# Optimization experiments

Hardware: AMD Instinct MI355X
Metric: run time of the kernel (lower is better)

Reference implementation:

```python
import jax, jax.numpy as jnp
import numpy as np

B, T, P, W = 32, 4096, 512, 1024  # batch, time, param_size, width


def setup_inputs() -> dict:
    key = jax.random.key(0)
    ks = jax.random.split(key, 9)
    lim = 1.0 / np.sqrt(W).astype(np.float32)
    lim = float(lim)
    u = lambda k, shape, l: jax.random.uniform(k, shape, minval=-l, maxval=l, dtype=jnp.float32)
    a = jax.random.normal(ks[0], (B, T, P), dtype=jnp.float32)
    h0 = u(ks[1], (W,), lim)
    weight_ih = u(ks[2], (3 * W, P), lim)
    weight_hh = u(ks[3], (3 * W, W), lim)
    bias = u(ks[4], (3 * W,), lim)
    bias_n = u(ks[5], (W,), lim)
    lim_o = float(1.0 / np.sqrt(W))
    w_out = u(ks[6], (P, W), lim_o)
    b_out = u(ks[7], (P,), lim_o)
    return {"a": a, "h0": h0, "weight_ih": weight_ih, "weight_hh": weight_hh,
            "bias": bias, "bias_n": bias_n, "w_out": w_out, "b_out": b_out}


def _encode(a, h0, weight_ih, weight_hh, bias, bias_n, w_out, b_out):
    # Precompute input gates for all steps (big GEMM, hoisted out of the scan).
    # ig: [B, T, 3W]
    ig = jnp.einsum('btp,gp->btg', a, weight_ih) + bias

    def step(h, ig_t):
        # h: [B, W], ig_t: [B, 3W]
        hg = h @ weight_hh.T                       # [B, 3W]
        ig_r, ig_z, ig_n = jnp.split(ig_t, 3, axis=-1)
        hg_r, hg_z, hg_n = jnp.split(hg, 3, axis=-1)
        r = jax.nn.sigmoid(ig_r + hg_r)
        z = jax.nn.sigmoid(ig_z + hg_z)
        n = jnp.tanh(ig_n + r * (hg_n + bias_n))
        h_new = n + z * (h - n)                    # equinox GRUCell update
        return h_new, h_new

    h_init = jnp.broadcast_to(h0, (a.shape[0], h0.shape[0]))
    # scan over time (reverse), batched inside: xs [T, B, 3W]
    _, hs = jax.lax.scan(step, h_init, jnp.swapaxes(ig, 0, 1), reverse=True)
    hs = jnp.swapaxes(hs, 0, 1)                    # [B, T, W]
    return hs @ w_out.T + b_out                    # [B, T, P]


def reference(a, h0, weight_ih, weight_hh, bias, bias_n, w_out, b_out):
    return _encode(a, h0, weight_ih, weight_hh, bias, bias_n, w_out, b_out)
```

## Files before the change

### kernel.cpp

```cpp
#include <hip/hip_runtime.h>
#include <cstddef>

#define TT 4096
#define PP 512
#define WW 1024

using u32 = unsigned;
using u64 = unsigned long long;
using u16 = unsigned short;

typedef short short8 __attribute__((ext_vector_type(8)));
typedef float f32x4 __attribute__((ext_vector_type(4)));

__device__ __forceinline__ u32 bfround(float f) {
    u32 u = __float_as_uint(f);
    return (u + 0x7fffu + ((u >> 16) & 1u)) >> 16;
}
__device__ __forceinline__ float bf2f(u32 q) { return __uint_as_float(q << 16); }
__device__ __forceinline__ float bflo(u32 q) { return __uint_as_float(q << 16); }
__device__ __forceinline__ float bfhi(u32 q) { return __uint_as_float(q & 0xffff0000u); }

#define LDA64(p)    __hip_atomic_load((p),  __ATOMIC_RELAXED, __HIP_MEMORY_SCOPE_AGENT)
#define STA64(p, v) __hip_atomic_store((p), (v), __ATOMIC_RELAXED, __HIP_MEMORY_SCOPE_AGENT)
#define LDA32(p)    __hip_atomic_load((p),  __ATOMIC_RELAXED, __HIP_MEMORY_SCOPE_AGENT)
#define STA32(p, v) __hip_atomic_store((p), (v), __ATOMIC_RELAXED, __HIP_MEMORY_SCOPE_AGENT)
#define STA16(p, v) __hip_atomic_store((p), (v), __ATOMIC_RELAXED, __HIP_MEMORY_SCOPE_AGENT)

__global__ __launch_bounds__(256, 2) void a2bf_t(const float* __restrict__ a,
                                                 u16* __restrict__ abf2) {
    __shared__ u16 sh[32][528];

    const int t   = blockIdx.x;
    const int tid = threadIdx.x;

    {
        const int b = tid >> 3, seg = tid & 7;
        const float* ap = &a[((size_t)b * TT + t) * PP + seg * 64];
        #pragma unroll
        for (int j = 0; j < 16; ++j) {
            float4 v = *(const float4*)&ap[j * 4];
            uint2 w;
            w.x = bfround(v.x) | (bfround(v.y) << 16);
            w.y = bfround(v.z) | (bfround(v.w) << 16);
            *(uint2*)&sh[b][seg * 64 + j * 4] = w;
        }
    }
    __syncthreads();
    {
        const int d = tid >> 2, bq = tid & 3;
        #pragma unroll
        for (int bb = 0; bb < 8; ++bb) {
            const int b = bq * 8 + bb;
            uint4 v = *(const uint4*)&sh[b][d * 8];
            *(uint4*)&abf2[(((size_t)t * 64 + d) * 32 + b) * 8] = v;
        }
    }
}

__global__ __launch_bounds__(768, 1) void ig_prepass9(
    const u16* __restrict__ abf2, const float* __restrict__ Wih,
    const float* __restrict__ bias, char* __restrict__ igbase)
{
    const int gp  = blockIdx.x;
    const int t0  = blockIdx.y * 64;
    const int tid = threadIdx.x;
    const int lane = tid & 63;
    const int wid  = tid >> 6;
    const int lq   = lane >> 4;
    const int bcol = lane & 15;

    short8 af[2][16];
    float  bi[2][4];
    int    gWGv[2], slotv[2];
    #pragma unroll
    for (int rt2 = 0; rt2 < 2; ++rt2) {
        const int rowb = gp * 384 + rt2 * 192 + wid * 16;
        const float* wr = &Wih[(size_t)(rowb + bcol) * PP + lq * 8];
        #pragma unroll
        for (int s = 0; s < 16; ++s) {
            float t8[8];
            *(float4*)&t8[0] = *(const float4*)&wr[s * 32];
            *(float4*)&t8[4] = *(const float4*)&wr[s * 32 + 4];
            #pragma unroll
            for (int j = 0; j < 8; ++j) af[rt2][s][j] = (short)bfround(t8[j]);
        }
        const int grow0 = rowb + lq * 4;
        #pragma unroll
        for (int r = 0; r < 4; ++r) bi[rt2][r] = bias[grow0 + r];
        const int gate = grow0 >> 10, w = grow0 & 1023;
        gWGv[rt2]  = w >> 4;
        slotv[rt2] = gate * 16 + (w & 15);
    }

    for (int ct = 0; ct < 128; ++ct) {
        const int t = t0 + (ct >> 1);
        const int b = (ct & 1) * 16 + bcol;
        const u16* bp = &abf2[(((size_t)t * 64 + lq) * 32 + b) * 8];
        f32x4 d0 = {0.f, 0.f, 0.f, 0.f}, d1 = {0.f, 0.f, 0.f, 0.f};
        #pragma unroll 4
        for (int s = 0; s < 16; ++s) {
            short8 bf = *(const short8*)&bp[(size_t)s * 4 * 256];
            d0 = __builtin_amdgcn_mfma_f32_16x16x32_bf16(af[0][s], bf, d0, 0, 0, 0);
            d1 = __builtin_amdgcn_mfma_f32_16x16x32_bf16(af[1][s], bf, d1, 0, 0, 0);
        }
        u32 l0 = bfround(d0[0] + bi[0][0]) | (bfround(d0[1] + bi[0][1]) << 16);
        u32 h0_ = bfround(d0[2] + bi[0][2]) | (bfround(d0[3] + bi[0][3]) << 16);
        u32 l1 = bfround(d1[0] + bi[1][0]) | (bfround(d1[1] + bi[1][1]) << 16);
        u32 h1_ = bfround(d1[2] + bi[1][2]) | (bfround(d1[3] + bi[1][3]) << 16);
        *(u64*)(igbase + (((size_t)t * 64 + gWGv[0]) * 1536 + (size_t)b * 48 + slotv[0]) * 2) = (u64)l0 | ((u64)h0_ << 32);
        *(u64*)(igbase + (((size_t)t * 64 + gWGv[1]) * 1536 + (size_t)b * 48 + slotv[1]) * 2) = (u64)l1 | ((u64)h1_ << 32);
    }
}

__global__ __launch_bounds__(768, 1) void ig_prepass16(
    const float* __restrict__ a, const float* __restrict__ Wih,
    const float* __restrict__ bias, char* __restrict__ igbase)
{
    const int gp   = blockIdx.x;
    const int t0   = blockIdx.y * 64;
    const int tid  = threadIdx.x;
    const int lane = tid & 63;
    const int wid  = tid >> 6;
    const int growb = gp * 192 + wid * 16;

    short8 afrag[16];
    float  biasv[4];
    {
        const float* wr = &Wih[(size_t)(growb + (lane & 15)) * PP + (lane >> 4) * 8];
        #pragma unroll
        for (int s = 0; s < 16; ++s) {
            float t8[8];
            *(float4*)&t8[0] = *(const float4*)&wr[s * 32];
            *(float4*)&t8[4] = *(const float4*)&wr[s * 32 + 4];
            #pragma unroll
            for (int j = 0; j < 8; ++j) afrag[s][j] = (short)bfround(t8[j]);
        }
        #pragma unroll
        for (int r = 0; r < 4; ++r) biasv[r] = bias[growb + (lane >> 4) * 4 + r];
    }
    const int grow0 = growb + (lane >> 4) * 4;
    const int gate  = grow0 >> 10;
    const int w     = grow0 & 1023;
    const int gWG   = w >> 4;
    const int slot  = gate * 16 + (w & 15);
    const int bcol  = lane & 15;

    for (int ct = 0; ct < 128; ++ct) {
        const int t = t0 + (ct >> 1);
        const int b = (ct & 1) * 16 + bcol;
        const float* ap = &a[((size_t)b * TT + t) * PP + (lane >> 4) * 8];
        f32x4 d = {0.f, 0.f, 0.f, 0.f};
        #pragma unroll 4
        for (int s = 0; s < 16; ++s) {
            float4 lo = *(const float4*)&ap[s * 32];
            float4 hi = *(const float4*)&ap[s * 32 + 4];
            short8 bfv;
            bfv[0] = (short)((__float_as_uint(lo.x) + 0x8000u) >> 16);
            bfv[1] = (short)((__float_as_uint(lo.y) + 0x8000u) >> 16);
            bfv[2] = (short)((__float_as_uint(lo.z) + 0x8000u) >> 16);
            bfv[3] = (short)((__float_as_uint(lo.w) + 0x8000u) >> 16);
            bfv[4] = (short)((__float_as_uint(hi.x) + 0x8000u) >> 16);
            bfv[5] = (short)((__float_as_uint(hi.y) + 0x8000u) >> 16);
            bfv[6] = (short)((__float_as_uint(hi.z) + 0x8000u) >> 16);
            bfv[7] = (short)((__float_as_uint(hi.w) + 0x8000u) >> 16);
            d = __builtin_amdgcn_mfma_f32_16x16x32_bf16(afrag[s], bfv, d, 0, 0, 0);
        }
        u32 lo32 = bfround(d[0] + biasv[0]) | (bfround(d[1] + biasv[1]) << 16);
        u32 hi32 = bfround(d[2] + biasv[2]) | (bfround(d[3] + biasv[3]) << 16);
        *(u64*)(igbase + (((size_t)t * 64 + gWG) * 1536 + (size_t)b * 48 + slot) * 2) =
            (u64)lo32 | ((u64)hi32 << 32);
    }
}

__global__ __launch_bounds__(768, 1) void gru_scan4(
    const float* __restrict__ h0v, const float* __restrict__ Whh,
    const float* __restrict__ bias_n, const float* __restrict__ Wout,
    const float* __restrict__ bout, const char* __restrict__ igbase,
    float* __restrict__ out, u64* __restrict__ bufA, u64* __restrict__ bufB,
    u32* __restrict__ flags)
{
    __shared__ float sPreH[4][48][2][17];
    __shared__ float sOutP[4][16][18];
    __shared__ __align__(8) u64 sIgRaw[384];

    const int g    = blockIdx.x;
    const int tid  = threadIdx.x;
    const int lane = tid & 63;
    const int wid  = tid >> 6;
    const int p0   = (g >> 1) * 16;
    const int pb0  = (g & 1) * 16;

    short8 frag[24];
    if (wid < 8) {
        const int kq = wid & 3;
        #pragma unroll
        for (int gate = 0; gate < 3; ++gate)
            #pragma unroll
            for (int s = 0; s < 8; ++s) {
                const float* wr = &Whh[(size_t)(gate * WW + g * 16 + (lane & 15)) * WW
                                       + (kq * 8 + s) * 32 + (lane >> 4) * 8];
                float t8[8];
                *(float4*)&t8[0] = *(const float4*)&wr[0];
                *(float4*)&t8[4] = *(const float4*)&wr[4];
                short8 v;
                #pragma unroll
                for (int j = 0; j < 8; ++j) v[j] = (short)bfround(t8[j]);
                frag[gate * 8 + s] = v;
            }
    } else {
        const int kq3 = wid - 8;
        #pragma unroll
        for (int s = 0; s < 8; ++s) {
            const float* wr = &Wout[(size_t)(p0 + (lane & 15)) * WW
                                    + (kq3 * 8 + s) * 32 + (lane >> 4) * 8];
            float t8[8];
            *(float4*)&t8[0] = *(const float4*)&wr[0];
            *(float4*)&t8[4] = *(const float4*)&wr[4];
            short8 v;
            #pragma unroll
            for (int j = 0; j < 8; ++j) v[j] = (short)bfround(t8[j]);
            frag[s] = v;
        }
    }

    float h_own = 0.f, bnv = 0.f;
    int gwl = 0, gb = 0; u32 hidx16 = 0;
    if (tid >= 256) {
        const int idx = tid - 256;
        gwl = idx & 15; gb = idx >> 4;
        h_own = h0v[g * 16 + gwl];
        bnv   = bias_n[g * 16 + gwl];
        const int w_abs = g * 16 + gwl;
        const int ip = (w_abs >> 3) * 64 + 2 * gb + ((w_abs >> 2) & 1);
        hidx16 = 4 * ip + (w_abs & 3);
        STA16(&((u16*)bufA)[hidx16], (u16)bfround(h_own));
    }
    const float boutp = (tid < 256) ? bout[p0 + (tid & 15)] : 0.f;

    const int fo_hh = (lane >> 4) * 32 + ((wid >> 2) & 1) * 16 + (lane & 15);
    const int fo_p3 = (lane >> 4) * 32 + pb0 + (lane & 15);

    u64* hcur = bufA;
    u64* hnxt = bufB;
    u32 kk = 1;

    for (int t = TT - 1; t >= 0; --t) {
        if (t < TT - 2 && tid < 256) {
            const int p = tid & 15, b = tid >> 4;
            float s_ = boutp;
            #pragma unroll
            for (int cc = 0; cc < 4; ++cc) s_ += sOutP[cc][p][b];
            out[((size_t)(pb0 + b) * TT + (t + 2)) * PP + p0 + p] = s_;
        }
        if (wid >= 4) asm volatile("s_waitcnt vmcnt(0)" ::: "memory");
        __syncthreads();
        if (tid == 0) STA32(&flags[g * 16], kk);

        u64 igr = 0;
        if (tid < 384) igr = *(const u64*)(igbase + ((size_t)t * 64 + g) * 3072 + tid * 8);

        for (;;) {
            u32 v = LDA32(&flags[lane * 16]);
            if (__all((int)(v - kk) >= 0)) break;
            __builtin_amdgcn_s_sleep(1);
        }
        asm volatile("" ::: "memory");

        if (wid < 8) {
            const int kq = wid & 3;
            f32x4 c0 = {0.f,0.f,0.f,0.f}, c1 = {0.f,0.f,0.f,0.f}, c2 = {0.f,0.f,0.f,0.f};
            #pragma unroll
            for (int s = 0; s < 8; ++s) {
                const int ss = kq * 8 + s;
                const u64 q0 = LDA64(&hcur[2 * (ss * 128 + fo_hh)]);
                const u64 q1 = LDA64(&hcur[2 * (ss * 128 + fo_hh) + 1]);
                union { u64 q[2]; short8 v; } uu; uu.q[0] = q0; uu.q[1] = q1;
                c0 = __builtin_amdgcn_mfma_f32_16x16x32_bf16(frag[s],      uu.v, c0, 0, 0, 0);
                c1 = __builtin_amdgcn_mfma_f32_16x16x32_bf16(frag[8 + s],  uu.v, c1, 0, 0, 0);
                c2 = __builtin_amdgcn_mfma_f32_16x16x32_bf16(frag[16 + s], uu.v, c2, 0, 0, 0);
            }
            const int bt = wid >> 2, r0 = (lane >> 4) * 4, col = lane & 15;
            #pragma unroll
            for (int r = 0; r < 4; ++r) {
                sPreH[kq][r0 + r][bt][col]      = c0[r];
                sPreH[kq][16 + r0 + r][bt][col] = c1[r];
                sPreH[kq][32 + r0 + r][bt][col] = c2[r];
            }
        } else {
            const int kq3 = wid - 8;
            f32x4 d = {0.f, 0.f, 0.f, 0.f};
            #pragma unroll
            for (int s = 0; s < 8; ++s) {
                const int ss = kq3 * 8 + s;
                const u64 q0 = LDA64(&hcur[2 * (ss * 128 + fo_p3)]);
                const u64 q1 = LDA64(&hcur[2 * (ss * 128 + fo_p3) + 1]);
                union { u64 q[2]; short8 v; } uu; uu.q[0] = q0; uu.q[1] = q1;
                d = __builtin_amdgcn_mfma_f32_16x16x32_bf16(frag[s], uu.v, d, 0, 0, 0);
            }
            const int r0 = (lane >> 4) * 4, col = lane & 15;
            #pragma unroll
            for (int r = 0; r < 4; ++r) sOutP[kq3][r0 + r][col] = d[r];
        }
        if (tid < 384) sIgRaw[tid] = igr;
        __syncthreads();

        if (tid >= 256) {
            const u16* sIgU = (const u16*)sIgRaw;
            const float ig_r = bf2f(sIgU[gb * 48 + gwl]);
            const float ig_z = bf2f(sIgU[gb * 48 + 16 + gwl]);
            const float ig_n = bf2f(sIgU[gb * 48 + 32 + gwl]);
            const int bh = gb >> 4, bc = gb & 15;
            const float hg_r = sPreH[0][gwl][bh][bc] + sPreH[1][gwl][bh][bc]
                             + sPreH[2][gwl][bh][bc] + sPreH[3][gwl][bh][bc];
            const float hg_z = sPreH[0][16 + gwl][bh][bc] + sPreH[1][16 + gwl][bh][bc]
                             + sPreH[2][16 + gwl][bh][bc] + sPreH[3][16 + gwl][bh][bc];
            const float hg_n = sPreH[0][32 + gwl][bh][bc] + sPreH[1][32 + gwl][bh][bc]
                             + sPreH[2][32 + gwl][bh][bc] + sPreH[3][32 + gwl][bh][bc];
            const float rr = __builtin_amdgcn_rcpf(1.f + __expf(-(ig_r + hg_r)));
            const float zz = __builtin_amdgcn_rcpf(1.f + __expf(-(ig_z + hg_z)));
            const float xn = ig_n + rr * (hg_n + bnv);
            const float nn = 2.f * __builtin_amdgcn_rcpf(1.f + __expf(-2.f * xn)) - 1.f;
            h_own = nn + zz * (h_own - nn);
            STA16(&((u16*)hnxt)[hidx16], (u16)bfround(h_own));
        }

        u64* tmp = hcur; hcur = hnxt; hnxt = tmp;
        ++kk;
    }

    if (tid < 256) {
        const int p = tid & 15, b = tid >> 4;
        float s_ = boutp;
        #pragma unroll
        for (int cc = 0; cc < 4; ++cc) s_ += sOutP[cc][p][b];
        out[((size_t)(pb0 + b) * TT + 1) * PP + p0 + p] = s_;
    }
    if (wid >= 4) asm volatile("s_waitcnt vmcnt(0)" ::: "memory");
    __syncthreads();
    if (tid == 0) STA32(&flags[g * 16], kk);
    if (wid >= 8) {
        for (;;) {
            u32 v = LDA32(&flags[lane * 16]);
            if (__all((int)(v - kk) >= 0)) break;
            __builtin_amdgcn_s_sleep(1);
        }
        asm volatile("" ::: "memory");
        const int kq3 = wid - 8;
        f32x4 d = {0.f, 0.f, 0.f, 0.f};
        #pragma unroll
        for (int s = 0; s < 8; ++s) {
            const int ss = kq3 * 8 + s;
            const u64 q0 = LDA64(&hcur[2 * (ss * 128 + fo_p3)]);
            const u64 q1 = LDA64(&hcur[2 * (ss * 128 + fo_p3) + 1]);
            union { u64 q[2]; short8 v; } uu; uu.q[0] = q0; uu.q[1] = q1;
            d = __builtin_amdgcn_mfma_f32_16x16x32_bf16(frag[s], uu.v, d, 0, 0, 0);
        }
        const int r0 = (lane >> 4) * 4, col = lane & 15;
        #pragma unroll
        for (int r = 0; r < 4; ++r) sOutP[kq3][r0 + r][col] = d[r];
    }
    __syncthreads();
    if (tid < 256) {
        const int p = tid & 15, b = tid >> 4;
        const float s_ = boutp + sOutP[0][p][b] + sOutP[1][p][b]
                               + sOutP[2][p][b] + sOutP[3][p][b];
        out[((size_t)(pb0 + b) * TT) * PP + p0 + p] = s_;
    }
}

__device__ __forceinline__ void grid_barrier32(u32* leaf, u32* root, u32 rtarget, int g) {
    asm volatile("s_waitcnt vmcnt(0)" ::: "memory");
    __syncthreads();
    if (threadIdx.x == 0) {
        u32 old = __hip_atomic_fetch_add(&leaf[(g & 7) * 16], 1u,
                                         __ATOMIC_RELAXED, __HIP_MEMORY_SCOPE_AGENT);
        if ((old & 31u) == 31u)
            __hip_atomic_fetch_add(root, 1u, __ATOMIC_RELAXED, __HIP_MEMORY_SCOPE_AGENT);
        while (__hip_atomic_load(root, __ATOMIC_RELAXED, __HIP_MEMORY_SCOPE_AGENT) < rtarget)
            __builtin_amdgcn_s_sleep(2);
    }
    __syncthreads();
}

__global__ __launch_bounds__(768, 1) void gru_scan_fb(
    const float* __restrict__ a, const float* __restrict__ h0,
    const float* __restrict__ Wih, const float* __restrict__ Whh,
    const float* __restrict__ bias, const float* __restrict__ bias_n,
    const float* __restrict__ Wout, const float* __restrict__ bout,
    float* __restrict__ out, u64* __restrict__ hbufA, u64* __restrict__ hbufB,
    u32* __restrict__ leaf, u32* __restrict__ root)
{
    __shared__ float sWhh[12][WW];
    __shared__ __align__(16) u64 sh[8192];
    __shared__ float sPreH[2][12][32];
    __shared__ float sIg[2][2][12][32];
    __shared__ float sOutPart[12][64];

    const int g   = blockIdx.x;
    const int tid = threadIdx.x;
    const int w0  = g * 4;

    for (int i = tid; i < 12 * (WW / 4); i += 768) {
        int row_ = i / (WW / 4);
        int k4_  = i - row_ * (WW / 4);
        int gr   = (row_ >> 2) * WW + w0 + (row_ & 3);
        *(float4*)&sWhh[row_][k4_ * 4] = *(const float4*)&Whh[(size_t)gr * WW + k4_ * 4];
    }
    const int  half = (tid >= 384) ? 1 : 0;
    const int  sub  = tid - half * 384;
    const int  b1   = sub & 31;
    const int  row  = sub >> 5;
    const int  grow = (row >> 2) * WW + w0 + (row & 3);
    const float biasv = (half == 0) ? bias[grow] : 0.0f;

    float ho0 = 0.f, ho1 = 0.f, ho2 = 0.f, ho3 = 0.f;
    float bn0 = 0.f, bn1 = 0.f, bn2 = 0.f, bn3 = 0.f;
    if (tid < 32) {
        ho0 = h0[w0 + 0]; ho1 = h0[w0 + 1]; ho2 = h0[w0 + 2]; ho3 = h0[w0 + 3];
        bn0 = bias_n[w0 + 0]; bn1 = bias_n[w0 + 1]; bn2 = bias_n[w0 + 2]; bn3 = bias_n[w0 + 3];
        u32 lo = bfround(ho0) | (bfround(ho1) << 16);
        u32 hi = bfround(ho2) | (bfround(ho3) << 16);
        STA64(&hbufA[g * 32 + tid], (u64)lo | ((u64)hi << 32));
    }
    const int  p0  = (g & 31) * 16;
    const int  b0  = (g >> 5) * 4;
    const int  o   = tid & 63;
    const int  c   = tid >> 6;
    const int  p3p = p0 + (o & 15);
    const int  p3b = b0 + (o >> 4);
    const float boutv = bout[p3p];

    auto ihdot = [&](int t_, int pbuf) {
        const float4* __restrict__ arow = (const float4*)&a[((size_t)b1 * TT + t_) * PP];
        const float4* __restrict__ wrow = (const float4*)&Wih[(size_t)grow * PP];
        const int p40 = half * 64;
        float4 acc = {0.f, 0.f, 0.f, 0.f};
        #pragma unroll 8
        for (int p4 = 0; p4 < 64; ++p4) {
            float4 av = arow[p40 + p4];
            float4 wv = wrow[p40 + p4];
            acc.x += av.x * wv.x; acc.y += av.y * wv.y;
            acc.z += av.z * wv.z; acc.w += av.w * wv.w;
        }
        sIg[pbuf][half][row][b1] = (acc.x + acc.y) + (acc.z + acc.w) + biasv;
    };
    auto p3partials = [&]() {
        const float4* __restrict__ wrow = (const float4*)&Wout[(size_t)p3p * WW];
        float4 acc = {0.f, 0.f, 0.f, 0.f};
        for (int k4 = c; k4 < WW / 4; k4 += 12) {
            u64 pk = sh[k4 * 32 + p3b];
            float4 wv = wrow[k4];
            acc.x += bflo((u32)pk) * wv.x;
            acc.y += bfhi((u32)pk) * wv.y;
            acc.z += bflo((u32)(pk >> 32)) * wv.z;
            acc.w += bfhi((u32)(pk >> 32)) * wv.w;
        }
        sOutPart[c][o] = (acc.x + acc.y) + (acc.z + acc.w);
    };

    ihdot(TT - 1, 1);
    u32 rtarget = 8;
    grid_barrier32(leaf, root, rtarget, g);
    u64* hcur = hbufA;
    u64* hnxt = hbufB;

    for (int t = TT - 1; t >= 0; --t) {
        const int par = t & 1;
        u64 r0, r1, r2, r3, r4, r5, r6, r7, r8, r9, r10 = 0;
        #define LDH(J) LDA64(&hcur[tid + (J) * 768])
        r0 = LDH(0); r1 = LDH(1); r2 = LDH(2); r3 = LDH(3); r4 = LDH(4);
        r5 = LDH(5); r6 = LDH(6); r7 = LDH(7); r8 = LDH(8); r9 = LDH(9);
        if (tid < 512) r10 = LDH(10);
        #undef LDH
        if (t > 0) ihdot(t - 1, par ^ 1);
        sh[tid] = r0;          sh[tid + 768] = r1;   sh[tid + 1536] = r2;
        sh[tid + 2304] = r3;   sh[tid + 3072] = r4;  sh[tid + 3840] = r5;
        sh[tid + 4608] = r6;   sh[tid + 5376] = r7;  sh[tid + 6144] = r8;
        sh[tid + 6912] = r9;
        if (tid < 512) sh[tid + 7680] = r10;
        __syncthreads();
        {
            const int k40 = half * 128;
            float4 acc = {0.f, 0.f, 0.f, 0.f};
            #pragma unroll 4
            for (int k4 = 0; k4 < 128; ++k4) {
                u64 pk = sh[(k40 + k4) * 32 + b1];
                float4 wv = *(const float4*)&sWhh[row][(k40 + k4) * 4];
                acc.x += bflo((u32)pk) * wv.x;
                acc.y += bfhi((u32)pk) * wv.y;
                acc.z += bflo((u32)(pk >> 32)) * wv.z;
                acc.w += bfhi((u32)(pk >> 32)) * wv.w;
            }
            sPreH[half][row][b1] = (acc.x + acc.y) + (acc.z + acc.w);
        }
        if (t < TT - 1) p3partials();
        __syncthreads();
        if (tid < 32) {
            const int b = tid;
            float hn0, hn1, hn2, hn3;
            {
                float rr = 1.f / (1.f + __expf(-(sIg[par][0][0][b] + sIg[par][1][0][b] + sPreH[0][0][b] + sPreH[1][0][b])));
                float zz = 1.f / (1.f + __expf(-(sIg[par][0][4][b] + sIg[par][1][4][b] + sPreH[0][4][b] + sPreH[1][4][b])));
                float nn = tanhf(sIg[par][0][8][b] + sIg[par][1][8][b] + rr * (sPreH[0][8][b] + sPreH[1][8][b] + bn0));
                hn0 = nn + zz * (ho0 - nn); ho0 = hn0;
            }
            {
                float rr = 1.f / (1.f + __expf(-(sIg[par][0][1][b] + sIg[par][1][1][b] + sPreH[0][1][b] + sPreH[1][1][b])));
                float zz = 1.f / (1.f + __expf(-(sIg[par][0][5][b] + sIg[par][1][5][b] + sPreH[0][5][b] + sPreH[1][5][b])));
                float nn = tanhf(sIg[par][0][9][b] + sIg[par][1][9][b] + rr * (sPreH[0][9][b] + sPreH[1][9][b] + bn1));
                hn1 = nn + zz * (ho1 - nn); ho1 = hn1;
            }
            {
                float rr = 1.f / (1.f + __expf(-(sIg[par][0][2][b] + sIg[par][1][2][b] + sPreH[0][2][b] + sPreH[1][2][b])));
                float zz = 1.f / (1.f + __expf(-(sIg[par][0][6][b] + sIg[par][1][6][b] + sPreH[0][6][b] + sPreH[1][6][b])));
                float nn = tanhf(sIg[par][0][10][b] + sIg[par][1][10][b] + rr * (sPreH[0][10][b] + sPreH[1][10][b] + bn2));
                hn2 = nn + zz * (ho2 - nn); ho2 = hn2;
            }
            {
                float rr = 1.f / (1.f + __expf(-(sIg[par][0][3][b] + sIg[par][1][3][b] + sPreH[0][3][b] + sPreH[1][3][b])));
                float zz = 1.f / (1.f + __expf(-(sIg[par][0][7][b] + sIg[par][1][7][b] + sPreH[0][7][b] + sPreH[1][7][b])));
                float nn = tanhf(sIg[par][0][11][b] + sIg[par][1][11][b] + rr * (sPreH[0][11][b] + sPreH[1][11][b] + bn3));
                hn3 = nn + zz * (ho3 - nn); ho3 = hn3;
            }
            u32 lo = bfround(hn0) | (bfround(hn1) << 16);
            u32 hi = bfround(hn2) | (bfround(hn3) << 16);
            STA64(&hnxt[g * 32 + tid], (u64)lo | ((u64)hi << 32));
        }
        if (t < TT - 1 && tid < 64) {
            float s_ = boutv;
            #pragma unroll
            for (int cc = 0; cc < 12; ++cc) s_ += sOutPart[cc][o];
            out[((size_t)p3b * TT + (t + 1)) * PP + p3p] = s_;
        }
        rtarget += 8;
        grid_barrier32(leaf, root, rtarget, g);
        u64* tmp = hcur; hcur = hnxt; hnxt = tmp;
    }
    {
        u64 r0, r1, r2, r3, r4, r5, r6, r7, r8, r9, r10 = 0;
        #define LDH(J) LDA64(&hcur[tid + (J) * 768])
        r0 = LDH(0); r1 = LDH(1); r2 = LDH(2); r3 = LDH(3); r4 = LDH(4);
        r5 = LDH(5); r6 = LDH(6); r7 = LDH(7); r8 = LDH(8); r9 = LDH(9);
        if (tid < 512) r10 = LDH(10);
        #undef LDH
        sh[tid] = r0;          sh[tid + 768] = r1;   sh[tid + 1536] = r2;
        sh[tid + 2304] = r3;   sh[tid + 3072] = r4;  sh[tid + 3840] = r5;
        sh[tid + 4608] = r6;   sh[tid + 5376] = r7;  sh[tid + 6144] = r8;
        sh[tid + 6912] = r9;
        if (tid < 512) sh[tid + 7680] = r10;
        __syncthreads();
        p3partials();
        __syncthreads();
        if (tid < 64) {
            float s_ = boutv;
            #pragma unroll
            for (int cc = 0; cc < 12; ++cc) s_ += sOutPart[cc][o];
            out[((size_t)p3b * TT) * PP + p3p] = s_;
        }
    }
}

extern "C" void kernel_launch(void* const* d_in, const int* in_sizes, int n_in,
                              void* d_out, int out_size, void* d_ws, size_t ws_size,
                              hipStream_t stream) {
    const float* a      = (const float*)d_in[0];
    const float* h0     = (const float*)d_in[1];
    const float* Wih    = (const float*)d_in[2];
    const float* Whh    = (const float*)d_in[3];
    const float* bias   = (const float*)d_in[4];
    const float* bias_n = (const float*)d_in[5];
    const float* Wout   = (const float*)d_in[6];
    const float* bout   = (const float*)d_in[7];
    float* out = (float*)d_out;

    const size_t IG_BYTES   = (size_t)TT * 64 * 3072;
    const size_t ABF2_BYTES = (size_t)TT * 64 * 32 * 8 * 2;
    const size_t NEED_FULL  = IG_BYTES + ABF2_BYTES + 2 * 65536 + 4096;
    const size_t NEED_MID   = IG_BYTES + 2 * 65536 + 4096;

    if (ws_size >= NEED_FULL) {
        char* igbase = (char*)d_ws;
        u16*  abf2   = (u16*)((char*)d_ws + IG_BYTES);
        u64*  bufA   = (u64*)((char*)d_ws + IG_BYTES + ABF2_BYTES);
        u64*  bufB   = bufA + 8192;
        u32*  flags  = (u32*)((char*)d_ws + IG_BYTES + ABF2_BYTES + 2 * 65536);
        hipMemsetAsync(flags, 0, 4096, stream);
        hipLaunchKernelGGL(a2bf_t, dim3(TT), dim3(256), 0, stream, a, abf2);
        hipLaunchKernelGGL(ig_prepass9, dim3(8, 64), dim3(768), 0, stream,
                           abf2, Wih, bias, igbase);
        void* args[] = {(void*)&h0, (void*)&Whh, (void*)&bias_n, (void*)&Wout,
                        (void*)&bout, (void*)&igbase, (void*)&out,
                        (void*)&bufA, (void*)&bufB, (void*)&flags};
        hipLaunchCooperativeKernel((void*)gru_scan4, dim3(64), dim3(768),
                                   args, 0, stream);
    } else if (ws_size >= NEED_MID) {
        char* igbase = (char*)d_ws;
        u64*  bufA   = (u64*)((char*)d_ws + IG_BYTES);
        u64*  bufB   = bufA + 8192;
        u32*  flags  = (u32*)((char*)d_ws + IG_BYTES + 2 * 65536);
        hipMemsetAsync(flags, 0, 4096, stream);
        hipLaunchKernelGGL(ig_prepass16, dim3(16, 64), dim3(768), 0, stream,
                           a, Wih, bias, igbase);
        void* args[] = {(void*)&h0, (void*)&Whh, (void*)&bias_n, (void*)&Wout,
                        (void*)&bout, (void*)&igbase, (void*)&out,
                        (void*)&bufA, (void*)&bufB, (void*)&flags};
        hipLaunchCooperativeKernel((void*)gru_scan4, dim3(64), dim3(768),
                                   args, 0, stream);
    } else {
        u64* hA   = (u64*)d_ws;
        u64* hB   = hA + 8192;
        u32* leaf = (u32*)((char*)d_ws + 2 * 65536);
        u32* root = leaf + 8 * 16;
        hipMemsetAsync(leaf, 0, 1024, stream);
        void* args[] = {(void*)&a, (void*)&h0, (void*)&Wih, (void*)&Whh,
                        (void*)&bias, (void*)&bias_n, (void*)&Wout, (void*)&bout,
                        (void*)&out, (void*)&hA, (void*)&hB, (void*)&leaf, (void*)&root};
        hipLaunchCooperativeKernel((void*)gru_scan_fb, dim3(256), dim3(768),
                                   args, 0, stream);
    }
}
```

Before: 19.97 ms.

## Restructure GRU scan sync with split per-wave flags and staged ig prepass stores

The input-gate prepass now assigns one 16-row gate tile per block, stages results for two timesteps in shared memory, and writes each timestep's ig slice as contiguous coalesced 64-bit stores instead of scattered ones. In the recurrent scan, gate threads each handle four hidden units and publish packed 64-bit h values. Two waves now publish per-block progress flags right after their own stores, which removes the block-wide barrier before the flag. The output projection write is moved after the gate phase, so the per-step critical path has fewer syncs. The cost is fewer active gate threads, more serial work per gate thread, and extra shared-memory barriers in the prepass.

```diff
diff --git a/kernel.cpp b/kernel.cpp
--- a/kernel.cpp
+++ b/kernel.cpp
@@ -32,7 +32,6 @@
 
     const int t   = blockIdx.x;
     const int tid = threadIdx.x;
-
     {
         const int b = tid >> 3, seg = tid & 7;
         const float* ap = &a[((size_t)b * TT + t) * PP + seg * 64];
@@ -57,58 +56,61 @@
     }
 }
 
-__global__ __launch_bounds__(768, 1) void ig_prepass9(
+__global__ __launch_bounds__(768, 1) void ig_prepass10(
     const u16* __restrict__ abf2, const float* __restrict__ Wih,
     const float* __restrict__ bias, char* __restrict__ igbase)
 {
-    const int gp  = blockIdx.x;
-    const int t0  = blockIdx.y * 64;
+    __shared__ __align__(8) u16 sIg[2][32][48];
+
+    const int gWG = blockIdx.x;
+    const int t0  = blockIdx.y * 128;
     const int tid = threadIdx.x;
     const int lane = tid & 63;
     const int wid  = tid >> 6;
+    const int tpar = wid / 6;
+    const int t6   = wid % 6;
+    const int st   = t6 >> 1;
+    const int bh   = t6 & 1;
     const int lq   = lane >> 4;
     const int bcol = lane & 15;
 
-    short8 af[2][16];
-    float  bi[2][4];
-    int    gWGv[2], slotv[2];
-    #pragma unroll
-    for (int rt2 = 0; rt2 < 2; ++rt2) {
-        const int rowb = gp * 384 + rt2 * 192 + wid * 16;
-        const float* wr = &Wih[(size_t)(rowb + bcol) * PP + lq * 8];
+    short8 af[16];
+    float  bi[4];
+    {
+        const float* wr = &Wih[(size_t)(st * WW + gWG * 16 + bcol) * PP + lq * 8];
         #pragma unroll
         for (int s = 0; s < 16; ++s) {
             float t8[8];
             *(float4*)&t8[0] = *(const float4*)&wr[s * 32];
             *(float4*)&t8[4] = *(const float4*)&wr[s * 32 + 4];
             #pragma unroll
-            for (int j = 0; j < 8; ++j) af[rt2][s][j] = (short)bfround(t8[j]);
-        }
-        const int grow0 = rowb + lq * 4;
-        #pragma unroll
-        for (int r = 0; r < 4; ++r) bi[rt2][r] = bias[grow0 + r];
-        const int gate = grow0 >> 10, w = grow0 & 1023;
-        gWGv[rt2]  = w >> 4;
-        slotv[rt2] = gate * 16 + (w & 15);
-    }
-
-    for (int ct = 0; ct < 128; ++ct) {
-        const int t = t0 + (ct >> 1);
-        const int b = (ct & 1) * 16 + bcol;
-        const u16* bp = &abf2[(((size_t)t * 64 + lq) * 32 + b) * 8];
-        f32x4 d0 = {0.f, 0.f, 0.f, 0.f}, d1 = {0.f, 0.f, 0.f, 0.f};
+            for (int j = 0; j < 8; ++j) af[s][j] = (short)bfround(t8[j]);
+        }
+        #pragma unroll
+        for (int r = 0; r < 4; ++r) bi[r] = bias[st * WW + gWG * 16 + lq * 4 + r];
+    }
+
+    for (int it = 0; it < 64; ++it) {
+        const int t = t0 + it * 2 + tpar;
+        const u16* bp = &abf2[(((size_t)t * 64 + lq) * 32 + (bh * 16 + bcol)) * 8];
+        f32x4 d = {0.f, 0.f, 0.f, 0.f};
         #pragma unroll 4
         for (int s = 0; s < 16; ++s) {
             short8 bf = *(const short8*)&bp[(size_t)s * 4 * 256];
-            d0 = __builtin_amdgcn_mfma_f32_16x16x32_bf16(af[0][s], bf, d0, 0, 0, 0);
-            d1 = __builtin_amdgcn_mfma_f32_16x16x32_bf16(af[1][s], bf, d1, 0, 0, 0);
-        }
-        u32 l0 = bfround(d0[0] + bi[0][0]) | (bfround(d0[1] + bi[0][1]) << 16);
-        u32 h0_ = bfround(d0[2] + bi[0][2]) | (bfround(d0[3] + bi[0][3]) << 16);
-        u32 l1 = bfround(d1[0] + bi[1][0]) | (bfround(d1[1] + bi[1][1]) << 16);
-        u32 h1_ = bfround(d1[2] + bi[1][2]) | (bfround(d1[3] + bi[1][3]) << 16);
-        *(u64*)(igbase + (((size_t)t * 64 + gWGv[0]) * 1536 + (size_t)b * 48 + slotv[0]) * 2) = (u64)l0 | ((u64)h0_ << 32);
-        *(u64*)(igbase + (((size_t)t * 64 + gWGv[1]) * 1536 + (size_t)b * 48 + slotv[1]) * 2) = (u64)l1 | ((u64)h1_ << 32);
+            d = __builtin_amdgcn_mfma_f32_16x16x32_bf16(af[s], bf, d, 0, 0, 0);
+        }
+        u32 lo = bfround(d[0] + bi[0]) | (bfround(d[1] + bi[1]) << 16);
+        u32 hi = bfround(d[2] + bi[2]) | (bfround(d[3] + bi[3]) << 16);
+        *(u64*)&sIg[tpar][bh * 16 + bcol][st * 16 + lq * 4] = (u64)lo | ((u64)hi << 32);
+        __syncthreads();
+        {
+            const int tp2 = tid / 384;
+            const int off = tid - tp2 * 384;
+            const int tt  = t0 + it * 2 + tp2;
+            ((u64*)(igbase + ((size_t)tt * 64 + gWG) * 3072))[off] =
+                ((const u64*)&sIg[tp2][0][0])[off];
+        }
+        __syncthreads();
     }
 }
 
@@ -172,7 +174,7 @@
     }
 }
 
-__global__ __launch_bounds__(768, 1) void gru_scan4(
+__global__ __launch_bounds__(768, 1) void gru_scan5(
     const float* __restrict__ h0v, const float* __restrict__ Whh,
     const float* __restrict__ bias_n, const float* __restrict__ Wout,
     const float* __restrict__ bout, const char* __restrict__ igbase,
@@ -223,20 +225,31 @@
         }
     }
 
-    float h_own = 0.f, bnv = 0.f;
-    int gwl = 0, gb = 0; u32 hidx16 = 0;
-    if (tid >= 256) {
+    const bool isGate = (tid >= 256 && tid < 384);
+    float h_own[4] = {0.f, 0.f, 0.f, 0.f};
+    float bnv[4]   = {0.f, 0.f, 0.f, 0.f};
+    int   q = 0, b_ = 0;
+    u32   pubIdx = 0;
+    if (isGate) {
         const int idx = tid - 256;
-        gwl = idx & 15; gb = idx >> 4;
-        h_own = h0v[g * 16 + gwl];
-        bnv   = bias_n[g * 16 + gwl];
-        const int w_abs = g * 16 + gwl;
-        const int ip = (w_abs >> 3) * 64 + 2 * gb + ((w_abs >> 2) & 1);
-        hidx16 = 4 * ip + (w_abs & 3);
-        STA16(&((u16*)bufA)[hidx16], (u16)bfround(h_own));
-    }
+        q  = idx & 3;
+        b_ = idx >> 2;
+        #pragma unroll
+        for (int j = 0; j < 4; ++j) {
+            h_own[j] = h0v[g * 16 + q * 4 + j];
+            bnv[j]   = bias_n[g * 16 + q * 4 + j];
+        }
+        pubIdx = (u32)(g * 128 + 2 * ((q >> 1) * 32 + b_) + (q & 1));
+        u32 lo = bfround(h_own[0]) | (bfround(h_own[1]) << 16);
+        u32 hi = bfround(h_own[2]) | (bfround(h_own[3]) << 16);
+        STA64(&bufA[pubIdx], (u64)lo | ((u64)hi << 32));
+    }
+    if (wid == 4 || wid == 5) {
+        asm volatile("s_waitcnt vmcnt(0)" ::: "memory");
+        if (lane == 0) STA32(&flags[g * 16 + (wid - 4)], 1u);
+    }
+
     const float boutp = (tid < 256) ? bout[p0 + (tid & 15)] : 0.f;
-
     const int fo_hh = (lane >> 4) * 32 + ((wid >> 2) & 1) * 16 + (lane & 15);
     const int fo_p3 = (lane >> 4) * 32 + pb0 + (lane & 15);
 
@@ -245,23 +258,15 @@
     u32 kk = 1;
 
     for (int t = TT - 1; t >= 0; --t) {
-        if (t < TT - 2 && tid < 256) {
-            const int p = tid & 15, b = tid >> 4;
-            float s_ = boutp;
-            #pragma unroll
-            for (int cc = 0; cc < 4; ++cc) s_ += sOutP[cc][p][b];
-            out[((size_t)(pb0 + b) * TT + (t + 2)) * PP + p0 + p] = s_;
-        }
-        if (wid >= 4) asm volatile("s_waitcnt vmcnt(0)" ::: "memory");
-        __syncthreads();
-        if (tid == 0) STA32(&flags[g * 16], kk);
+        __syncthreads();
 
         u64 igr = 0;
         if (tid < 384) igr = *(const u64*)(igbase + ((size_t)t * 64 + g) * 3072 + tid * 8);
 
         for (;;) {
-            u32 v = LDA32(&flags[lane * 16]);
-            if (__all((int)(v - kk) >= 0)) break;
+            u64 v = LDA64((const u64*)&flags[lane * 16]);
+            const u32 lo = (u32)v, hi = (u32)(v >> 32);
+            if (__all(((int)(lo - kk) >= 0) && ((int)(hi - kk) >= 0))) break;
             __builtin_amdgcn_s_sleep(1);
         }
         asm volatile("" ::: "memory");
@@ -274,7 +279,7 @@
                 const int ss = kq * 8 + s;
                 const u64 q0 = LDA64(&hcur[2 * (ss * 128 + fo_hh)]);
                 const u64 q1 = LDA64(&hcur[2 * (ss * 128 + fo_hh) + 1]);
-                union { u64 q[2]; short8 v; } uu; uu.q[0] = q0; uu.q[1] = q1;
+                union { u64 qq[2]; short8 v; } uu; uu.qq[0] = q0; uu.qq[1] = q1;
                 c0 = __builtin_amdgcn_mfma_f32_16x16x32_bf16(frag[s],      uu.v, c0, 0, 0, 0);
                 c1 = __builtin_amdgcn_mfma_f32_16x16x32_bf16(frag[8 + s],  uu.v, c1, 0, 0, 0);
                 c2 = __builtin_amdgcn_mfma_f32_16x16x32_bf16(frag[16 + s], uu.v, c2, 0, 0, 0);
@@ -286,7 +291,7 @@
                 sPreH[kq][16 + r0 + r][bt][col] = c1[r];
                 sPreH[kq][32 + r0 + r][bt][col] = c2[r];
             }
-        } else {
+        } else if (t < TT - 1) {
             const int kq3 = wid - 8;
             f32x4 d = {0.f, 0.f, 0.f, 0.f};
             #pragma unroll
@@ -294,7 +299,7 @@
                 const int ss = kq3 * 8 + s;
                 const u64 q0 = LDA64(&hcur[2 * (ss * 128 + fo_p3)]);
                 const u64 q1 = LDA64(&hcur[2 * (ss * 128 + fo_p3) + 1]);
-                union { u64 q[2]; short8 v; } uu; uu.q[0] = q0; uu.q[1] = q1;
+                union { u64 qq[2]; short8 v; } uu; uu.qq[0] = q0; uu.qq[1] = q1;
                 d = __builtin_amdgcn_mfma_f32_16x16x32_bf16(frag[s], uu.v, d, 0, 0, 0);
             }
             const int r0 = (lane >> 4) * 4, col = lane & 15;
@@ -304,44 +309,55 @@
         if (tid < 384) sIgRaw[tid] = igr;
         __syncthreads();
 
-        if (tid >= 256) {
+        if (isGate) {
             const u16* sIgU = (const u16*)sIgRaw;
-            const float ig_r = bf2f(sIgU[gb * 48 + gwl]);
-            const float ig_z = bf2f(sIgU[gb * 48 + 16 + gwl]);
-            const float ig_n = bf2f(sIgU[gb * 48 + 32 + gwl]);
-            const int bh = gb >> 4, bc = gb & 15;
-            const float hg_r = sPreH[0][gwl][bh][bc] + sPreH[1][gwl][bh][bc]
-                             + sPreH[2][gwl][bh][bc] + sPreH[3][gwl][bh][bc];
-            const float hg_z = sPreH[0][16 + gwl][bh][bc] + sPreH[1][16 + gwl][bh][bc]
-                             + sPreH[2][16 + gwl][bh][bc] + sPreH[3][16 + gwl][bh][bc];
-            const float hg_n = sPreH[0][32 + gwl][bh][bc] + sPreH[1][32 + gwl][bh][bc]
-                             + sPreH[2][32 + gwl][bh][bc] + sPreH[3][32 + gwl][bh][bc];
-            const float rr = __builtin_amdgcn_rcpf(1.f + __expf(-(ig_r + hg_r)));
-            const float zz = __builtin_amdgcn_rcpf(1.f + __expf(-(ig_z + hg_z)));
-            const float xn = ig_n + rr * (hg_n + bnv);
-            const float nn = 2.f * __builtin_amdgcn_rcpf(1.f + __expf(-2.f * xn)) - 1.f;
-            h_own = nn + zz * (h_own - nn);
-            STA16(&((u16*)hnxt)[hidx16], (u16)bfround(h_own));
+            const int bh = b_ >> 4, bc = b_ & 15;
+            u32 lo = 0, hi = 0;
+            #pragma unroll
+            for (int j = 0; j < 4; ++j) {
+                const int gwl = q * 4 + j;
+                const float ig_r = bf2f(sIgU[b_ * 48 + gwl]);
+                const float ig_z = bf2f(sIgU[b_ * 48 + 16 + gwl]);
+                const float ig_n = bf2f(sIgU[b_ * 48 + 32 + gwl]);
+                const float hg_r = sPreH[0][gwl][bh][bc] + sPreH[1][gwl][bh][bc]
+                                 + sPreH[2][gwl][bh][bc] + sPreH[3][gwl][bh][bc];
+                const float hg_z = sPreH[0][16 + gwl][bh][bc] + sPreH[1][16 + gwl][bh][bc]
+                                 + sPreH[2][16 + gwl][bh][bc] + sPreH[3][16 + gwl][bh][bc];
+                const float hg_n = sPreH[0][32 + gwl][bh][bc] + sPreH[1][32 + gwl][bh][bc]
+                                 + sPreH[2][32 + gwl][bh][bc] + sPreH[3][32 + gwl][bh][bc];
+                const float rr = __builtin_amdgcn_rcpf(1.f + __expf(-(ig_r + hg_r)));
+                const float zz = __builtin_amdgcn_rcpf(1.f + __expf(-(ig_z + hg_z)));
+                const float xn = ig_n + rr * (hg_n + bnv[j]);
+                const float nn = 2.f * __builtin_amdgcn_rcpf(1.f + __expf(-2.f * xn)) - 1.f;
+                h_own[j] = nn + zz * (h_own[j] - nn);
+                const u32 bv = bfround(h_own[j]);
+                if (j == 0) lo = bv;
+                else if (j == 1) lo |= bv << 16;
+                else if (j == 2) hi = bv;
+                else hi |= bv << 16;
+            }
+            STA64(&hnxt[pubIdx], (u64)lo | ((u64)hi << 32));
+        } else if (tid < 256 && t < TT - 1) {
+            const int p = tid & 15, b = tid >> 4;
+            const float s_ = boutp + sOutP[0][p][b] + sOutP[1][p][b]
+                                   + sOutP[2][p][b] + sOutP[3][p][b];
+            out[((size_t)(pb0 + b) * TT + (t + 1)) * PP + p0 + p] = s_;
+        }
+        if (wid == 4 || wid == 5) {
+            asm volatile("s_waitcnt vmcnt(0)" ::: "memory");
+            if (lane == 0) STA32(&flags[g * 16 + (wid - 4)], kk + 1u);
         }
 
         u64* tmp = hcur; hcur = hnxt; hnxt = tmp;
         ++kk;
     }
 
-    if (tid < 256) {
-        const int p = tid & 15, b = tid >> 4;
-        float s_ = boutp;
-        #pragma unroll
-        for (int cc = 0; cc < 4; ++cc) s_ += sOutP[cc][p][b];
-        out[((size_t)(pb0 + b) * TT + 1) * PP + p0 + p] = s_;
-    }
-    if (wid >= 4) asm volatile("s_waitcnt vmcnt(0)" ::: "memory");
     __syncthreads();
-    if (tid == 0) STA32(&flags[g * 16], kk);
     if (wid >= 8) {
         for (;;) {
-            u32 v = LDA32(&flags[lane * 16]);
-            if (__all((int)(v - kk) >= 0)) break;
+            u64 v = LDA64((const u64*)&flags[lane * 16]);
+            const u32 lo = (u32)v, hi = (u32)(v >> 32);
+            if (__all(((int)(lo - kk) >= 0) && ((int)(hi - kk) >= 0))) break;
             __builtin_amdgcn_s_sleep(1);
         }
         asm volatile("" ::: "memory");
@@ -352,7 +368,7 @@
             const int ss = kq3 * 8 + s;
             const u64 q0 = LDA64(&hcur[2 * (ss * 128 + fo_p3)]);
             const u64 q1 = LDA64(&hcur[2 * (ss * 128 + fo_p3) + 1]);
-            union { u64 q[2]; short8 v; } uu; uu.q[0] = q0; uu.q[1] = q1;
+            union { u64 qq[2]; short8 v; } uu; uu.qq[0] = q0; uu.qq[1] = q1;
             d = __builtin_amdgcn_mfma_f32_16x16x32_bf16(frag[s], uu.v, d, 0, 0, 0);
         }
         const int r0 = (lane >> 4) * 4, col = lane & 15;
@@ -586,12 +602,12 @@
         u32*  flags  = (u32*)((char*)d_ws + IG_BYTES + ABF2_BYTES + 2 * 65536);
         hipMemsetAsync(flags, 0, 4096, stream);
         hipLaunchKernelGGL(a2bf_t, dim3(TT), dim3(256), 0, stream, a, abf2);
-        hipLaunchKernelGGL(ig_prepass9, dim3(8, 64), dim3(768), 0, stream,
+        hipLaunchKernelGGL(ig_prepass10, dim3(64, 32), dim3(768), 0, stream,
                            abf2, Wih, bias, igbase);
         void* args[] = {(void*)&h0, (void*)&Whh, (void*)&bias_n, (void*)&Wout,
                         (void*)&bout, (void*)&igbase, (void*)&out,
                         (void*)&bufA, (void*)&bufB, (void*)&flags};
-        hipLaunchCooperativeKernel((void*)gru_scan4, dim3(64), dim3(768),
+        hipLaunchCooperativeKernel((void*)gru_scan5, dim3(64), dim3(768),
                                    args, 0, stream);
     } else if (ws_size >= NEED_MID) {
         char* igbase = (char*)d_ws;
@@ -604,7 +620,7 @@
         void* args[] = {(void*)&h0, (void*)&Whh, (void*)&bias_n, (void*)&Wout,
                         (void*)&bout, (void*)&igbase, (void*)&out,
                         (void*)&bufA, (void*)&bufB, (void*)&flags};
-        hipLaunchCooperativeKernel((void*)gru_scan4, dim3(64), dim3(768),
+        hipLaunchCooperativeKernel((void*)gru_scan5, dim3(64), dim3(768),
                                    args, 0, stream);
     } else {
         u64* hA   = (u64*)d_ws;
```

Result: slower. 20.93 ms (+4.8%).
